# Performance work log

Measured on AMD Instinct MI355X. Metric: run time of the kernel, lower is better.

## Reference

```python
import jax, jax.numpy as jnp
import numpy as np
import math

B, IN_DIM, HID, OUT_DIM = 8192, 64, 256, 4096
N_STEPS = 20


def logx_and_kl(loga, logb, alpha):
    # logx = log(alpha*a + (1-alpha)*b); kl = KL(x || b)
    logx = jnp.logaddexp(loga + jnp.log(alpha), logb + jnp.log(1.0 - alpha))
    kl = jnp.sum(jnp.exp(logx) * (logx - logb), axis=-1, keepdims=True)
    return logx, kl


def dkl_dalpha(loga, logb, logx):
    a_minus_b = jnp.exp(loga) - jnp.exp(logb)
    return jnp.sum(a_minus_b * (logx - logb + 1.0), axis=-1, keepdims=True)


def findalphafork(loga, logb, k, n_steps=N_STEPS):
    def body(i, carry):
        alpha, bot, top = carry
        logx, kl = logx_and_kl(loga, logb, alpha)
        bot = jnp.where(k >= kl, alpha, bot)
        top = jnp.where(k <= kl, alpha, top)
        d = dkl_dalpha(loga, logb, logx)
        delta = (k - kl) / (d + 1e-12)
        alpha = jnp.clip(alpha + delta,
                         bot * (15.0 / 16.0) + top * (1.0 / 16.0),
                         bot * 0.5 + top * 0.5)
        return alpha, bot, top

    init = (jnp.ones_like(k), jnp.zeros_like(k), jnp.ones_like(k))
    alpha, _, _ = jax.lax.fori_loop(0, n_steps, body, init)
    return alpha


def kl_fixed_mixture(k, loga, logb):
    alpha = findalphafork(loga, logb, k)
    return logx_and_kl(loga, logb, alpha)


def setup_inputs() -> dict:
    key = jax.random.key(0)
    ks = jax.random.split(key, 10)
    x = jax.random.normal(ks[0], (B, IN_DIM), dtype=jnp.float32)
    kl_budget = jax.random.uniform(ks[1], (B, 1), dtype=jnp.float32)
    log_base_dist = jax.nn.log_softmax(
        jax.random.normal(ks[2], (B, OUT_DIM), dtype=jnp.float32), axis=-1)
    W0 = jax.random.normal(ks[3], (HID, IN_DIM + 1), dtype=jnp.float32) * (0.05 / math.sqrt(IN_DIM + 1))
    b0 = jax.random.normal(ks[4], (HID,), dtype=jnp.float32) * 0.01
    W1 = jax.random.normal(ks[5], (HID, HID), dtype=jnp.float32) * (1.0 / math.sqrt(HID))
    b1 = jax.random.normal(ks[6], (HID,), dtype=jnp.float32) * 0.01
    W2 = jax.random.normal(ks[7], (OUT_DIM + 1, HID), dtype=jnp.float32) * 0.01
    b2 = jax.random.normal(ks[8], (OUT_DIM + 1,), dtype=jnp.float32) * 0.01
    return {"x": x, "kl_budget": kl_budget, "log_base_dist": log_base_dist,
            "W0": W0, "b0": b0, "W1": W1, "b1": b1, "W2": W2, "b2": b2,
            "actions_left": 16}


def reference(x, kl_budget, log_base_dist, W0, b0, W1, b1, W2, b2, actions_left):
    h = jnp.concatenate([x, kl_budget], axis=-1)  # [B, IN_DIM+1]
    for i, (W, b) in enumerate(((W0, b0), (W1, b1), (W2, b2))):
        if i != 0:
            h = jnp.tanh(h)
        h = h @ W.T + b
    # n_versions_last_layer == 1 -> selected_x = h
    kl_target = jax.nn.sigmoid(h[:, :1] - math.log(actions_left)) * kl_budget + 1e-6
    loga = h[:, 1:] + log_base_dist
    loga = loga - jnp.max(loga, axis=-1, keepdims=True)
    loga = loga - jax.nn.logsumexp(loga, axis=-1, keepdims=True)
    logx, kl_achieved = kl_fixed_mixture(kl_target, loga, log_base_dist)
    return jax.nn.softmax(logx, axis=-1), jnp.square(kl_achieved - kl_target)
```

## Files before the change

### kernel.cpp

```cpp
#include <hip/hip_runtime.h>
#include <hip/hip_bf16.h>
#include <math.h>

typedef float f32x4 __attribute__((ext_vector_type(4)));
typedef __bf16 bf16x8 __attribute__((ext_vector_type(8)));
typedef unsigned short ushort;

#define NROWS 8192
#define HID 256
#define NCOL 4096
#define NSTEPS 20

static __device__ inline float bf2f(ushort u) {
    union { unsigned int i; float f; } c; c.i = ((unsigned int)u) << 16; return c.f;
}
static __device__ inline ushort f2bf(float x) {
    __hip_bfloat16 h = __float2bfloat16(x);
    union { __hip_bfloat16 h; ushort u; } c; c.h = h; return c.u;
}
static __device__ inline void gload_lds16(const void* g, void* l) {
    __builtin_amdgcn_global_load_lds(
        (const __attribute__((address_space(1))) void*)g,
        (__attribute__((address_space(3))) void*)l, 16, 0, 0);
}

__global__ __launch_bounds__(256) void mlp01_kernel(
    const float* __restrict__ x, const float* __restrict__ klb,
    const float* __restrict__ W0, const float* __restrict__ b0,
    const float* __restrict__ W1, const float* __restrict__ b1,
    ushort* __restrict__ t_ext)
{
    __shared__ float xk[8][66];
    __shared__ float h0[8][HID];
    const int tid = threadIdx.x;
    const int r0 = blockIdx.x * 8;

    for (int f = tid; f < 8 * 64; f += 256) {
        int r = f >> 6, k = f & 63;
        xk[r][k] = x[(r0 + r) * 64 + k];
    }
    if (tid < 8) xk[tid][64] = klb[r0 + tid];
    __syncthreads();

    {
        float acc[8];
        float bb = b0[tid];
        #pragma unroll
        for (int r = 0; r < 8; r++) acc[r] = bb;
        for (int k = 0; k < 65; k++) {
            float w = W0[tid * 65 + k];
            #pragma unroll
            for (int r = 0; r < 8; r++) acc[r] += w * xk[r][k];
        }
        #pragma unroll
        for (int r = 0; r < 8; r++) h0[r][tid] = tanhf(acc[r]);
    }
    __syncthreads();
    {
        float acc[8];
        float bb = b1[tid];
        #pragma unroll
        for (int r = 0; r < 8; r++) acc[r] = bb;
        for (int k = 0; k < HID; k++) {
            float w = W1[tid * HID + k];
            #pragma unroll
            for (int r = 0; r < 8; r++) acc[r] += w * h0[r][k];
        }
        #pragma unroll
        for (int r = 0; r < 8; r++) {
            float v = tanhf(acc[r]);
            ushort hi = f2bf(v);
            float lo = v - bf2f(hi);
            size_t base = (size_t)(r0 + r) * 512;
            t_ext[base + tid] = hi;
            t_ext[base + 256 + tid] = f2bf(lo);
        }
    }
}

__global__ __launch_bounds__(256) void w2ext_kernel(const float* __restrict__ W2,
                                                    ushort* __restrict__ Bext)
{
    const int r = blockIdx.x, t = threadIdx.x;
    float v = W2[(size_t)(r + 1) * 256 + t];
    ushort hi = f2bf(v);
    float lo = v - bf2f(hi);
    Bext[(size_t)r * 512 + t] = hi;
    Bext[(size_t)r * 512 + 256 + t] = f2bf(lo);
}

__global__ __launch_bounds__(256) void kt_kernel(
    const ushort* __restrict__ t_ext, const float* __restrict__ W2,
    const float* __restrict__ b2, const float* __restrict__ klb,
    const int* __restrict__ AL, float* __restrict__ kt)
{
    const int w = threadIdx.x >> 6, lane = threadIdx.x & 63;
    const int r = blockIdx.x * 4 + w;
    const size_t base = (size_t)r * 512 + lane * 4;
    f32x4 wv = *(const f32x4*)&W2[lane * 4];
    float acc = 0.0f;
    #pragma unroll
    for (int j = 0; j < 4; j++) {
        float tv = bf2f(t_ext[base + j]) + bf2f(t_ext[base + 256 + j]);
        acc = fmaf(tv, wv[j], acc);
    }
    for (int off = 32; off; off >>= 1) acc += __shfl_down(acc, off);
    if (lane == 0) {
        float z = acc + b2[0] - logf((float)AL[0]);
        float sg = 1.0f / (1.0f + expf(-z));
        kt[r] = sg * klb[r] + 1e-6f;
    }
}

__global__ __launch_bounds__(256) void gemm2_mfma(
    const ushort* __restrict__ Aext, const ushort* __restrict__ Bext,
    const float* __restrict__ b2, float* __restrict__ h2out)
{
    __shared__ ushort As[128 * 64];
    __shared__ ushort Bs[128 * 64];
    const int tid = threadIdx.x;
    const int lane = tid & 63, w = tid >> 6;
    const int m0 = blockIdx.y * 128, c0 = blockIdx.x * 128;
    const int wm = w & 1, wn = w >> 1;

    f32x4 acc[4][4];
    #pragma unroll
    for (int i = 0; i < 4; i++)
        #pragma unroll
        for (int j = 0; j < 4; j++) acc[i][j] = (f32x4){0.f, 0.f, 0.f, 0.f};

    int sg_row[4], sg_c[4];
    #pragma unroll
    for (int s = 0; s < 4; s++) {
        int idx = (s * 4 + w) * 512 + lane * 8;
        int row = idx >> 6;
        int cp = (idx >> 3) & 7;
        sg_row[s] = row;
        sg_c[s] = cp ^ (row & 7);
    }

    for (int kt = 0; kt < 8; kt++) {
        const int k0 = kt * 64;
        #pragma unroll
        for (int s = 0; s < 4; s++) {
            gload_lds16(&Aext[(size_t)(m0 + sg_row[s]) * 512 + k0 + sg_c[s] * 8],
                        &As[(s * 4 + w) * 512]);
            gload_lds16(&Bext[(size_t)(c0 + sg_row[s]) * 512 + k0 + sg_c[s] * 8],
                        &Bs[(s * 4 + w) * 512]);
        }
        __syncthreads();
        #pragma unroll
        for (int kk = 0; kk < 2; kk++) {
            const int cA = kk * 4 + (lane >> 4);
            bf16x8 af[4], bfr[4];
            #pragma unroll
            for (int i = 0; i < 4; i++) {
                int mr = wm * 64 + i * 16 + (lane & 15);
                af[i] = *(const bf16x8*)&As[mr * 64 + ((cA ^ (mr & 7)) * 8)];
                int nr = wn * 64 + i * 16 + (lane & 15);
                bfr[i] = *(const bf16x8*)&Bs[nr * 64 + ((cA ^ (nr & 7)) * 8)];
            }
            #pragma unroll
            for (int i = 0; i < 4; i++)
                #pragma unroll
                for (int j = 0; j < 4; j++)
                    acc[i][j] = __builtin_amdgcn_mfma_f32_16x16x32_bf16(
                        af[i], bfr[j], acc[i][j], 0, 0, 0);
        }
        __syncthreads();
    }

    const int colb = c0 + wn * 64 + (lane & 15);
    #pragma unroll
    for (int j = 0; j < 4; j++) {
        float bias = b2[1 + colb + j * 16];
        #pragma unroll
        for (int i = 0; i < 4; i++) {
            int rr = m0 + wm * 64 + i * 16 + (lane >> 4) * 4;
            #pragma unroll
            for (int q = 0; q < 4; q++)
                h2out[(size_t)(rr + q) * 4096 + colb + j * 16] = acc[i][j][q] + bias;
        }
    }
}

__global__ __launch_bounds__(128) void solve_kernel(
    float* __restrict__ outbuf, const float* __restrict__ logb_g,
    const float* __restrict__ ktarr)
{
    __shared__ float red[8];
    const int tid = threadIdx.x;
    const int lane = tid & 63, w = tid >> 6;
    const int r = blockIdx.x;

    float amb[32];
    float eb[32];

    const float* rowA = outbuf + (size_t)r * 4096;
    const float* rowB = logb_g + (size_t)r * 4096;

    float s = 0.0f, t1 = 0.0f, c2 = 0.0f, seb = 0.0f;
    #pragma unroll
    for (int c = 0; c < 8; c++) {
        f32x4 av = *(const f32x4*)&rowA[c * 512 + tid * 4];
        f32x4 bv = *(const f32x4*)&rowB[c * 512 + tid * 4];
        #pragma unroll
        for (int j = 0; j < 4; j++) {
            int m = c * 4 + j;
            float e = __expf(av[j] + bv[j]);
            float b = __expf(bv[j]);
            amb[m] = e;
            eb[m] = b;
            s += e;
            t1 = fmaf(e, bv[j], t1);
            c2 = fmaf(b, bv[j], c2);
            seb += b;
        }
    }
    #pragma unroll
    for (int off = 1; off < 64; off <<= 1) {
        s   += __shfl_xor(s, off);
        t1  += __shfl_xor(t1, off);
        c2  += __shfl_xor(c2, off);
        seb += __shfl_xor(seb, off);
    }
    if (lane == 0) {
        red[w * 4 + 0] = s;  red[w * 4 + 1] = t1;
        red[w * 4 + 2] = c2; red[w * 4 + 3] = seb;
    }
    __syncthreads();
    s   = red[0] + red[4];
    t1  = red[1] + red[5];
    c2  = red[2] + red[6];
    seb = red[3] + red[7];
    __syncthreads();

    const float inv = 1.0f / s;
    const float C2 = c2;
    const float C3 = fmaf(inv, t1, -c2);
    const float C4 = (1.0f - seb) - C3;
    #pragma unroll
    for (int m = 0; m < 32; m++)
        amb[m] = fmaf(amb[m], inv, -eb[m]);

    const float k = ktarr[r];
    float alpha = 1.0f, bot = 0.0f, top = 1.0f;

    for (int it = 0; it < NSTEPS; it++) {
        float kacc = 0.0f, dacc = 0.0f;
        #pragma unroll
        for (int m = 0; m < 32; m++) {
            float xv = fmaf(alpha, amb[m], eb[m]);
            float lx = __logf(xv);
            kacc = fmaf(xv, lx, kacc);
            dacc = fmaf(amb[m], lx, dacc);
        }
        #pragma unroll
        for (int off = 1; off < 64; off <<= 1) {
            kacc += __shfl_xor(kacc, off);
            dacc += __shfl_xor(dacc, off);
        }
        if (lane == 0) { red[w * 2 + 0] = kacc; red[w * 2 + 1] = dacc; }
        __syncthreads();
        kacc = red[0] + red[2];
        dacc = red[1] + red[3];
        __syncthreads();

        float klc = kacc - C2 - alpha * C3;
        float dc  = dacc + C4;

        bot = (k >= klc) ? alpha : bot;
        top = (k <= klc) ? alpha : top;
        float delta = (k - klc) / (dc + 1e-12f);
        float lo = bot * (15.0f / 16.0f) + top * (1.0f / 16.0f);
        float hi = 0.5f * (bot + top);
        alpha = fminf(hi, fmaxf(lo, alpha + delta));
        if (top - bot < 1e-6f) break;
    }

    float spx = 0.0f, kacc = 0.0f;
    #pragma unroll
    for (int m = 0; m < 32; m++) {
        float xv = fmaf(alpha, amb[m], eb[m]);
        float lx = __logf(xv);
        spx += xv;
        kacc = fmaf(xv, lx, kacc);
    }
    #pragma unroll
    for (int off = 1; off < 64; off <<= 1) {
        spx  += __shfl_xor(spx, off);
        kacc += __shfl_xor(kacc, off);
    }
    if (lane == 0) { red[w * 2 + 0] = spx; red[w * 2 + 1] = kacc; }
    __syncthreads();
    spx  = red[0] + red[2];
    kacc = red[1] + red[3];

    const float skl = kacc - C2 - alpha * C3;
    const float invs = 1.0f / spx;

    float* orow = outbuf + (size_t)r * 4096;
    #pragma unroll
    for (int c = 0; c < 8; c++) {
        f32x4 o;
        #pragma unroll
        for (int j = 0; j < 4; j++)
            o[j] = fmaf(alpha, amb[c * 4 + j], eb[c * 4 + j]) * invs;
        *(f32x4*)&orow[c * 512 + tid * 4] = o;
    }
    if (tid == 0) {
        float d = skl - k;
        outbuf[(size_t)NROWS * NCOL + r] = d * d;
    }
}

extern "C" void kernel_launch(void* const* d_in, const int* in_sizes, int n_in,
                              void* d_out, int out_size, void* d_ws, size_t ws_size,
                              hipStream_t stream)
{
    const float* x    = (const float*)d_in[0];
    const float* klb  = (const float*)d_in[1];
    const float* logb = (const float*)d_in[2];
    const float* W0   = (const float*)d_in[3];
    const float* b0   = (const float*)d_in[4];
    const float* W1   = (const float*)d_in[5];
    const float* b1   = (const float*)d_in[6];
    const float* W2   = (const float*)d_in[7];
    const float* b2   = (const float*)d_in[8];
    const int*   AL   = (const int*)d_in[9];
    float* out = (float*)d_out;

    ushort* tws  = (ushort*)d_ws;
    ushort* Bext = tws + (size_t)8192 * 512;
    float*  kt   = (float*)(Bext + (size_t)4096 * 512);

    hipLaunchKernelGGL(mlp01_kernel, dim3(1024), dim3(256), 0, stream, x, klb, W0, b0, W1, b1, tws);
    hipLaunchKernelGGL(w2ext_kernel, dim3(4096), dim3(256), 0, stream, W2, Bext);
    hipLaunchKernelGGL(kt_kernel, dim3(2048), dim3(256), 0, stream, tws, W2, b2, klb, AL, kt);
    hipLaunchKernelGGL(gemm2_mfma, dim3(32, 64), dim3(256), 0, stream, tws, Bext, b2, out);
    hipLaunchKernelGGL(solve_kernel, dim3(8192), dim3(128), 0, stream, out, logb, kt);
}
```

Measured before the change: 192.3 us.

## Widen solve blocks to 256 threads and skip redundant final KL pass

```diff
diff --git a/kernel.cpp b/kernel.cpp
--- a/kernel.cpp
+++ b/kernel.cpp
@@ -184,26 +184,26 @@
     }
 }
 
-__global__ __launch_bounds__(128) void solve_kernel(
+__global__ __launch_bounds__(256) void solve_kernel(
     float* __restrict__ outbuf, const float* __restrict__ logb_g,
     const float* __restrict__ ktarr)
 {
-    __shared__ float red[8];
+    __shared__ float red[16];
     const int tid = threadIdx.x;
     const int lane = tid & 63, w = tid >> 6;
     const int r = blockIdx.x;
 
-    float amb[32];
-    float eb[32];
+    float amb[16];
+    float eb[16];
 
     const float* rowA = outbuf + (size_t)r * 4096;
     const float* rowB = logb_g + (size_t)r * 4096;
 
     float s = 0.0f, t1 = 0.0f, c2 = 0.0f, seb = 0.0f;
     #pragma unroll
-    for (int c = 0; c < 8; c++) {
-        f32x4 av = *(const f32x4*)&rowA[c * 512 + tid * 4];
-        f32x4 bv = *(const f32x4*)&rowB[c * 512 + tid * 4];
+    for (int c = 0; c < 4; c++) {
+        f32x4 av = *(const f32x4*)&rowA[c * 1024 + tid * 4];
+        f32x4 bv = *(const f32x4*)&rowB[c * 1024 + tid * 4];
         #pragma unroll
         for (int j = 0; j < 4; j++) {
             int m = c * 4 + j;
@@ -229,10 +229,10 @@
         red[w * 4 + 2] = c2; red[w * 4 + 3] = seb;
     }
     __syncthreads();
-    s   = red[0] + red[4];
-    t1  = red[1] + red[5];
-    c2  = red[2] + red[6];
-    seb = red[3] + red[7];
+    s   = red[0] + red[4] + red[8]  + red[12];
+    t1  = red[1] + red[5] + red[9]  + red[13];
+    c2  = red[2] + red[6] + red[10] + red[14];
+    seb = red[3] + red[7] + red[11] + red[15];
     __syncthreads();
 
     const float inv = 1.0f / s;
@@ -240,16 +240,18 @@
     const float C3 = fmaf(inv, t1, -c2);
     const float C4 = (1.0f - seb) - C3;
     #pragma unroll
-    for (int m = 0; m < 32; m++)
+    for (int m = 0; m < 16; m++)
         amb[m] = fmaf(amb[m], inv, -eb[m]);
 
     const float k = ktarr[r];
     float alpha = 1.0f, bot = 0.0f, top = 1.0f;
+    float a_eval = -1.0f, skl = 0.0f;
 
     for (int it = 0; it < NSTEPS; it++) {
+        a_eval = alpha;
         float kacc = 0.0f, dacc = 0.0f;
         #pragma unroll
-        for (int m = 0; m < 32; m++) {
+        for (int m = 0; m < 16; m++) {
             float xv = fmaf(alpha, amb[m], eb[m]);
             float lx = __logf(xv);
             kacc = fmaf(xv, lx, kacc);
@@ -262,12 +264,13 @@
         }
         if (lane == 0) { red[w * 2 + 0] = kacc; red[w * 2 + 1] = dacc; }
         __syncthreads();
-        kacc = red[0] + red[2];
-        dacc = red[1] + red[3];
+        kacc = red[0] + red[2] + red[4] + red[6];
+        dacc = red[1] + red[3] + red[5] + red[7];
         __syncthreads();
 
         float klc = kacc - C2 - alpha * C3;
         float dc  = dacc + C4;
+        skl = klc;
 
         bot = (k >= klc) ? alpha : bot;
         top = (k <= klc) ? alpha : top;
@@ -278,35 +281,32 @@
         if (top - bot < 1e-6f) break;
     }
 
-    float spx = 0.0f, kacc = 0.0f;
-    #pragma unroll
-    for (int m = 0; m < 32; m++) {
-        float xv = fmaf(alpha, amb[m], eb[m]);
-        float lx = __logf(xv);
-        spx += xv;
-        kacc = fmaf(xv, lx, kacc);
-    }
-    #pragma unroll
-    for (int off = 1; off < 64; off <<= 1) {
-        spx  += __shfl_xor(spx, off);
-        kacc += __shfl_xor(kacc, off);
-    }
-    if (lane == 0) { red[w * 2 + 0] = spx; red[w * 2 + 1] = kacc; }
-    __syncthreads();
-    spx  = red[0] + red[2];
-    kacc = red[1] + red[3];
-
-    const float skl = kacc - C2 - alpha * C3;
+    if (alpha != a_eval) {
+        float kacc = 0.0f;
+        #pragma unroll
+        for (int m = 0; m < 16; m++) {
+            float xv = fmaf(alpha, amb[m], eb[m]);
+            kacc = fmaf(xv, __logf(xv), kacc);
+        }
+        #pragma unroll
+        for (int off = 1; off < 64; off <<= 1) kacc += __shfl_xor(kacc, off);
+        if (lane == 0) red[w] = kacc;
+        __syncthreads();
+        kacc = red[0] + red[1] + red[2] + red[3];
+        skl = kacc - C2 - alpha * C3;
+    }
+
+    const float spx = fmaf(alpha, 1.0f - seb, seb);
     const float invs = 1.0f / spx;
 
     float* orow = outbuf + (size_t)r * 4096;
     #pragma unroll
-    for (int c = 0; c < 8; c++) {
+    for (int c = 0; c < 4; c++) {
         f32x4 o;
         #pragma unroll
         for (int j = 0; j < 4; j++)
             o[j] = fmaf(alpha, amb[c * 4 + j], eb[c * 4 + j]) * invs;
-        *(f32x4*)&orow[c * 512 + tid * 4] = o;
+        *(f32x4*)&orow[c * 1024 + tid * 4] = o;
     }
     if (tid == 0) {
         float d = skl - k;
@@ -338,5 +338,5 @@
     hipLaunchKernelGGL(w2ext_kernel, dim3(4096), dim3(256), 0, stream, W2, Bext);
     hipLaunchKernelGGL(kt_kernel, dim3(2048), dim3(256), 0, stream, tws, W2, b2, klb, AL, kt);
     hipLaunchKernelGGL(gemm2_mfma, dim3(32, 64), dim3(256), 0, stream, tws, Bext, b2, out);
-    hipLaunchKernelGGL(solve_kernel, dim3(8192), dim3(128), 0, stream, out, logb, kt);
-}
+    hipLaunchKernelGGL(solve_kernel, dim3(8192), dim3(256), 0, stream, out, logb, kt);
+}
```

Result: faster. 184.4 us (-4.1%).
